# Performance work log

Measured on AMD Instinct MI355X. Metric: run time of the kernel, lower is better.

Reference implementation:

```python
import jax, jax.numpy as jnp
import numpy as np

NEG_SLOPE = 0.2
EPS = 1e-16

def gatv2(x, edge_index, edge_attr, Wl, bl, We, att, bias):
    """PyG GATv2Conv, heads=1, share_weights=True, with edge_dim."""
    N = x.shape[0]
    h = x @ Wl + bl                      # [N, out] shared lin_l == lin_r
    src, dst = edge_index[0], edge_index[1]
    hj = h[src]                          # source (message) features [E, out]
    hi = h[dst]                          # target features [E, out]
    e = jax.nn.leaky_relu(hi + hj + edge_attr @ We, NEG_SLOPE)  # [E, out]
    score = e @ att                      # [E]
    # segment softmax over edges grouped by destination node
    smax = jax.ops.segment_max(score, dst, num_segments=N)
    ex = jnp.exp(score - smax[dst])
    denom = jax.ops.segment_sum(ex, dst, num_segments=N)
    alpha = ex / (denom[dst] + EPS)      # [E]
    out = jax.ops.segment_sum(hj * alpha[:, None], dst, num_segments=N)
    return out + bias


def setup_inputs() -> dict:
    key = jax.random.key(0)
    N, E = 50000, 800000
    D_IN, D_LAT, D_EDGE, N_ACT = 128, 128, 16, 32
    ks = jax.random.split(key, 16)
    s = 0.05
    inp = {
        "x": jax.random.normal(ks[0], (N, D_IN), jnp.float32),
        "edge_index": jax.random.randint(ks[1], (2, E), 0, N, jnp.int32),
        "edge_attr": jax.random.normal(ks[2], (E, D_EDGE), jnp.float32),
        # gnn_layer: D_IN -> D_LAT
        "Wl1": jax.random.normal(ks[3], (D_IN, D_LAT), jnp.float32) * s,
        "bl1": jnp.zeros((D_LAT,), jnp.float32),
        "We1": jax.random.normal(ks[4], (D_EDGE, D_LAT), jnp.float32) * s,
        "att1": jax.random.normal(ks[5], (D_LAT,), jnp.float32) * s,
        "bias1": jnp.zeros((D_LAT,), jnp.float32),
        # node_layer: D_LAT -> 1
        "Wl2": jax.random.normal(ks[6], (D_LAT, 1), jnp.float32) * s,
        "bl2": jnp.zeros((1,), jnp.float32),
        "We2": jax.random.normal(ks[7], (D_EDGE, 1), jnp.float32) * s,
        "att2": jax.random.normal(ks[8], (1,), jnp.float32) * s,
        "bias2": jnp.zeros((1,), jnp.float32),
        # action_layer: D_LAT -> N_ACT
        "Wl3": jax.random.normal(ks[9], (D_LAT, N_ACT), jnp.float32) * s,
        "bl3": jnp.zeros((N_ACT,), jnp.float32),
        "We3": jax.random.normal(ks[10], (D_EDGE, N_ACT), jnp.float32) * s,
        "att3": jax.random.normal(ks[11], (N_ACT,), jnp.float32) * s,
        "bias3": jnp.zeros((N_ACT,), jnp.float32),
    }
    return inp


def reference(x, edge_index, edge_attr,
              Wl1, bl1, We1, att1, bias1,
              Wl2, bl2, We2, att2, bias2,
              Wl3, bl3, We3, att3, bias3):
    latent = gatv2(x, edge_index, edge_attr, Wl1, bl1, We1, att1, bias1)          # [N, D_LAT]
    node_logits = gatv2(latent, edge_index, edge_attr, Wl2, bl2, We2, att2, bias2)[:, 0]  # [N]
    action_logits = gatv2(latent, edge_index, edge_attr, Wl3, bl3, We3, att3, bias3)      # [N, A]
    # categorical sampling with fixed key (deterministic reference)
    k1, k2 = jax.random.split(jax.random.key(42))
    node_sel = jax.random.categorical(k1, node_logits)
    node_lp = jax.nn.log_softmax(node_logits)[node_sel]
    act_logits_sel = action_logits[node_sel, :]
    action_sel = jax.random.categorical(k2, act_logits_sel)
    action_lp = jax.nn.log_softmax(act_logits_sel)[action_sel]
    return (node_sel, action_sel, node_lp + action_lp)
```

## Files before the change

### kernel.cpp

```cpp
#include <hip/hip_runtime.h>
#include <stdint.h>
#include <math.h>

#define NEG 0.2f
#define TINYF 1.1754943508222875e-38f

typedef float f4 __attribute__((ext_vector_type(4)));
typedef float f2 __attribute__((ext_vector_type(2)));

__host__ __device__ inline void threefry2x32(uint32_t k0, uint32_t k1,
                                             uint32_t x0, uint32_t x1,
                                             uint32_t* o0, uint32_t* o1) {
  uint32_t ks0 = k0, ks1 = k1, ks2 = k0 ^ k1 ^ 0x1BD11BDAu;
  x0 += ks0; x1 += ks1;
#define RR(r) { x0 += x1; x1 = (x1 << (r)) | (x1 >> (32 - (r))); x1 ^= x0; }
  RR(13) RR(15) RR(26) RR(6)
  x0 += ks1; x1 += ks2 + 1u;
  RR(17) RR(29) RR(16) RR(24)
  x0 += ks2; x1 += ks0 + 2u;
  RR(13) RR(15) RR(26) RR(6)
  x0 += ks0; x1 += ks1 + 3u;
  RR(17) RR(29) RR(16) RR(24)
  x0 += ks1; x1 += ks2 + 4u;
  RR(13) RR(15) RR(26) RR(6)
  x0 += ks2; x1 += ks0 + 5u;
#undef RR
  *o0 = x0; *o1 = x1;
}

__device__ inline float gumbel_part(uint32_t ka, uint32_t kb, uint32_t i) {
  uint32_t o0, o1;
  threefry2x32(ka, kb, 0u, i, &o0, &o1);
  uint32_t bits = o0 ^ o1;
  float f = __uint_as_float((bits >> 9) | 0x3f800000u) - 1.0f;
  float u = fmaxf(TINYF, f + TINYF);
  return -logf(-logf(u));
}

__global__ void count_kernel(const int* __restrict__ ei, int E, int* __restrict__ counts) {
  int e = blockIdx.x * blockDim.x + threadIdx.x;
  if (e < E) atomicAdd(&counts[ei[E + e]], 1);
}

#define SCB 256
__global__ __launch_bounds__(256) void scan_partial_kernel(const int* __restrict__ counts,
    int N, int chunk, int* __restrict__ bsum) {
  int b = blockIdx.x;
  int s0 = b * chunk, s1 = s0 + chunk; if (s1 > N) s1 = N;
  int tid = threadIdx.x;
  int v = 0;
  for (int i = s0 + tid; i < s1; i += 256) v += counts[i];
  __shared__ int red[256];
  red[tid] = v; __syncthreads();
  for (int s = 128; s; s >>= 1) { if (tid < s) red[tid] += red[tid + s]; __syncthreads(); }
  if (tid == 0) bsum[b] = red[0];
}

__global__ __launch_bounds__(256) void scan_offsets_kernel(const int* __restrict__ bsum,
    int* __restrict__ boff, int* __restrict__ row_start, int N) {
  int tid = threadIdx.x; int lane = tid & 63; int wv = tid >> 6;
  __shared__ int wsum[4];
  int v = bsum[tid];
  int incl = v;
#pragma unroll
  for (int off = 1; off < 64; off <<= 1) {
    int t = __shfl_up(incl, off);
    if (lane >= off) incl += t;
  }
  if (lane == 63) wsum[wv] = incl;
  __syncthreads();
  if (tid == 0) {
    int s = 0;
    for (int k = 0; k < 4; k++) { int t = wsum[k]; wsum[k] = s; s += t; }
    row_start[N] = s;
  }
  __syncthreads();
  boff[tid] = wsum[wv] + incl - v;
}

__global__ __launch_bounds__(256) void scan_apply_kernel(const int* __restrict__ counts,
    const int* __restrict__ boff, int N, int chunk,
    int* __restrict__ row_start, int* __restrict__ cursor) {
  int b = blockIdx.x;
  int s0 = b * chunk, s1 = s0 + chunk; if (s1 > N) s1 = N;
  int tid = threadIdx.x; int lane = tid & 63; int wv = tid >> 6;
  __shared__ int wsum[4];
  __shared__ int tot_s;
  __shared__ int base_s;
  if (tid == 0) base_s = boff[b];
  __syncthreads();
  for (int c0 = s0; c0 < s1; c0 += 256) {
    int i = c0 + tid;
    int v = (i < s1) ? counts[i] : 0;
    int incl = v;
#pragma unroll
    for (int off = 1; off < 64; off <<= 1) {
      int t = __shfl_up(incl, off);
      if (lane >= off) incl += t;
    }
    if (lane == 63) wsum[wv] = incl;
    __syncthreads();
    if (tid == 0) {
      int s = 0;
      for (int k = 0; k < 4; k++) { int t = wsum[k]; wsum[k] = s; s += t; }
      tot_s = s;
    }
    __syncthreads();
    int base = base_s;
    int excl = base + wsum[wv] + incl - v;
    if (i < s1) { row_start[i] = excl; cursor[i] = excl; }
    __syncthreads();
    if (tid == 0) base_s = base + tot_s;
    __syncthreads();
  }
}

__global__ void scatter_kernel(const int* __restrict__ ei, const float* __restrict__ ea,
                               int E, int* __restrict__ cursor,
                               int* __restrict__ src_csr, float* __restrict__ ea_csr) {
  int e = blockIdx.x * blockDim.x + threadIdx.x;
  if (e < E) {
    int d = ei[E + e];
    int p = atomicAdd(&cursor[d], 1);
    src_csr[p] = ei[e];
    const float4* s4 = (const float4*)&ea[(size_t)e * 16];
    float4* d4 = (float4*)&ea_csr[(size_t)p * 16];
    float4 t0 = s4[0], t1 = s4[1], t2 = s4[2], t3 = s4[3];
    d4[0] = t0; d4[1] = t1; d4[2] = t2; d4[3] = t3;
  }
}

__global__ __launch_bounds__(256) void gemm128_kernel(const float* __restrict__ X,
    const float* __restrict__ W, const float* __restrict__ bias,
    float* __restrict__ out, int M) {
  __shared__ float xs[128][33];
  int row0 = blockIdx.x * 32;
  int tid = threadIdx.x;
  for (int idx = tid; idx < 32 * 128; idx += 256) {
    int r = idx >> 7;
    int k = idx & 127;
    int row = row0 + r;
    xs[k][r] = (row < M) ? X[(size_t)row * 128 + k] : 0.0f;
  }
  __syncthreads();
  int tc = tid & 31, tr = tid >> 5;
  int c0 = tc * 4, r0 = tr * 4;
  float acc[4][4] = {};
#pragma unroll 4
  for (int k = 0; k < 128; k++) {
    float4 w = *(const float4*)&W[k * 128 + c0];
    float x0 = xs[k][r0], x1 = xs[k][r0 + 1], x2 = xs[k][r0 + 2], x3 = xs[k][r0 + 3];
    acc[0][0] += x0 * w.x; acc[0][1] += x0 * w.y; acc[0][2] += x0 * w.z; acc[0][3] += x0 * w.w;
    acc[1][0] += x1 * w.x; acc[1][1] += x1 * w.y; acc[1][2] += x1 * w.z; acc[1][3] += x1 * w.w;
    acc[2][0] += x2 * w.x; acc[2][1] += x2 * w.y; acc[2][2] += x2 * w.z; acc[2][3] += x2 * w.w;
    acc[3][0] += x3 * w.x; acc[3][1] += x3 * w.y; acc[3][2] += x3 * w.z; acc[3][3] += x3 * w.w;
  }
  float4 b4 = *(const float4*)&bias[c0];
  for (int r = 0; r < 4; r++) {
    int row = row0 + r0 + r;
    if (row < M) {
      float4 o;
      o.x = acc[r][0] + b4.x; o.y = acc[r][1] + b4.y;
      o.z = acc[r][2] + b4.z; o.w = acc[r][3] + b4.w;
      *(float4*)&out[(size_t)row * 128 + c0] = o;
    }
  }
}

__global__ __launch_bounds__(256) void gemm32_kernel(const float* __restrict__ X,
    const float* __restrict__ W, const float* __restrict__ bias,
    float* __restrict__ out, int M) {
  int t = blockIdx.x * 256 + threadIdx.x;
  int node = t >> 5, c = t & 31;
  if (node >= M) return;
  const float4* xp = (const float4*)&X[(size_t)node * 128];
  float acc = 0.f;
#pragma unroll
  for (int q = 0; q < 32; q++) {
    float4 x4 = xp[q];
    acc += x4.x * W[(q * 4 + 0) * 32 + c] + x4.y * W[(q * 4 + 1) * 32 + c]
         + x4.z * W[(q * 4 + 2) * 32 + c] + x4.w * W[(q * 4 + 3) * 32 + c];
  }
  out[(size_t)node * 32 + c] = acc + bias[c];
}

__global__ __launch_bounds__(256) void gemv_kernel(const float* __restrict__ X,
    const float* __restrict__ w, const float* __restrict__ b0,
    float* __restrict__ out, int M) {
  int wv = (blockIdx.x * 256 + threadIdx.x) >> 6;
  int lane = threadIdx.x & 63;
  if (wv >= M) return;
  float2 xv = *(const float2*)&X[(size_t)wv * 128 + lane * 2];
  float2 wvv = *(const float2*)&w[lane * 2];
  float v = xv.x * wvv.x + xv.y * wvv.y;
#pragma unroll
  for (int off = 32; off; off >>= 1) v += __shfl_xor(v, off);
  if (lane == 0) out[wv] = v + b0[0];
}

__global__ __launch_bounds__(256) void fused1_kernel(const float* __restrict__ h,
    const int* __restrict__ src_csr, const int* __restrict__ row_start,
    const float* __restrict__ ea_csr,
    const float* __restrict__ We, const float* __restrict__ att,
    const float* __restrict__ bias, float* __restrict__ out, int N) {
  __shared__ float WeS[2048];
  int tid = threadIdx.x;
  for (int i = tid; i < 2048; i += 256) WeS[i] = We[i];
  __syncthreads();
  int hw = (blockIdx.x * 256 + tid) >> 5;
  int lane = tid & 31;
  if (hw >= N) return;
  int c4 = lane * 4;
  const f4* W4 = (const f4*)WeS;
  f4 attv = *(const f4*)&att[c4];
  f4 bb = *(const f4*)&bias[c4];
  int start = row_start[hw];
  int deg = row_start[hw + 1] - start;
  if (deg == 0) {
    *(f4*)&out[(size_t)hw * 128 + c4] = bb;
    return;
  }
  f4 hi = *(const f4*)&h[(size_t)hw * 128 + c4];
  int s_l = (lane < deg) ? src_csr[start + lane] : 0;
  int dcap = deg < 32 ? deg : 32;
  const f4* eap = (const f4*)&ea_csr[(size_t)start * 16];
  float m = -INFINITY, l = 0.f;
  f4 acc = (f4)0.f;
  for (int j = 0; j < deg; j++) {
    int s = (j < dcap) ? __shfl(s_l, j, 32) : src_csr[start + j];
    f4 hj = *(const f4*)&h[(size_t)s * 128 + c4];
    f4 v = hi + hj;
#pragma unroll
    for (int q = 0; q < 4; q++) {
      f4 aq = eap[(size_t)j * 4 + q];
      v += aq.x * W4[(4 * q + 0) * 32 + lane];
      v += aq.y * W4[(4 * q + 1) * 32 + lane];
      v += aq.z * W4[(4 * q + 2) * 32 + lane];
      v += aq.w * W4[(4 * q + 3) * 32 + lane];
    }
    v.x = v.x >= 0.f ? v.x : NEG * v.x;
    v.y = v.y >= 0.f ? v.y : NEG * v.y;
    v.z = v.z >= 0.f ? v.z : NEG * v.z;
    v.w = v.w >= 0.f ? v.w : NEG * v.w;
    f4 pv = v * attv;
    float sc = (pv.x + pv.y) + (pv.z + pv.w);
#pragma unroll
    for (int off = 16; off; off >>= 1) sc += __shfl_xor(sc, off);
    float mn = fmaxf(m, sc);
    float scale = __expf(m - mn);
    float w = __expf(sc - mn);
    l = l * scale + w;
    acc = acc * scale + w * hj;
    m = mn;
  }
  float inv = 1.0f / (l + 1e-16f);
  f4 o = acc * inv + bb;
  *(f4*)&out[(size_t)hw * 128 + c4] = o;
}

__global__ __launch_bounds__(256) void fused23_kernel(
    const float* __restrict__ h3, const float* __restrict__ h2,
    const int* __restrict__ src_csr, const int* __restrict__ row_start,
    const float* __restrict__ ea_csr,
    const float* __restrict__ We3, const float* __restrict__ att3,
    const float* __restrict__ bias3, const float* __restrict__ We2,
    const float* __restrict__ att2, const float* __restrict__ bias2,
    float* __restrict__ out3, float* __restrict__ logits, int N) {
  __shared__ float We3S[512];
  __shared__ float att3S[32];
  __shared__ float We2S[16];
  int tid = threadIdx.x;
  for (int i = tid; i < 512; i += 256) We3S[i] = We3[i];
  if (tid < 32) att3S[tid] = att3[tid];
  if (tid < 16) We2S[tid] = We2[tid];
  __syncthreads();
  int wv = (blockIdx.x * 256 + tid) >> 6;
  int lane = tid & 63;
  if (wv >= N) return;
  int q4 = lane >> 4;
  int l16 = lane & 15;
  int c2 = l16 * 2;
  const f2* W3 = (const f2*)We3S;
  f2 at3 = *(const f2*)&att3S[c2];
  float a2s = att2[0];
  f2 bi3 = *(const f2*)&bias3[c2];
  int start = row_start[wv];
  int deg = row_start[wv + 1] - start;
  if (deg == 0) {
    if (lane < 16) *(f2*)&out3[(size_t)wv * 32 + c2] = bi3;
    if (lane == 0) logits[wv] = bias2[0];
    return;
  }
  f2 hi3 = *(const f2*)&h3[(size_t)wv * 32 + c2];
  float hi2 = h2[wv];
  int s_l = (lane < deg) ? src_csr[start + lane] : 0;
  int dcap = deg < 64 ? deg : 64;
  const float4* eap = (const float4*)&ea_csr[(size_t)start * 16];
  float m3 = -INFINITY, l3 = 0.f; f2 a3 = (f2)0.f;
  float m2 = -INFINITY, l2 = 0.f; float a2 = 0.f;
  for (int j = q4; j < deg; j += 4) {
    int s = (j < dcap) ? __shfl(s_l, j) : src_csr[start + j];
    f2 hj3 = *(const f2*)&h3[(size_t)s * 32 + c2];
    float h2s = h2[s];
    float4 c0 = eap[(size_t)j * 4 + 0];
    float4 c1 = eap[(size_t)j * 4 + 1];
    float4 cc2 = eap[(size_t)j * 4 + 2];
    float4 c3 = eap[(size_t)j * 4 + 3];
    f2 v = hi3 + hj3;
    v += c0.x * W3[0 * 16 + l16];  v += c0.y * W3[1 * 16 + l16];
    v += c0.z * W3[2 * 16 + l16];  v += c0.w * W3[3 * 16 + l16];
    v += c1.x * W3[4 * 16 + l16];  v += c1.y * W3[5 * 16 + l16];
    v += c1.z * W3[6 * 16 + l16];  v += c1.w * W3[7 * 16 + l16];
    v += cc2.x * W3[8 * 16 + l16]; v += cc2.y * W3[9 * 16 + l16];
    v += cc2.z * W3[10 * 16 + l16]; v += cc2.w * W3[11 * 16 + l16];
    v += c3.x * W3[12 * 16 + l16]; v += c3.y * W3[13 * 16 + l16];
    v += c3.z * W3[14 * 16 + l16]; v += c3.w * W3[15 * 16 + l16];
    v.x = v.x >= 0.f ? v.x : NEG * v.x;
    v.y = v.y >= 0.f ? v.y : NEG * v.y;
    float t3 = v.x * at3.x + v.y * at3.y;
#pragma unroll
    for (int off = 8; off; off >>= 1) t3 += __shfl_xor(t3, off);
    float v2 = hi2 + h2s;
    v2 += c0.x * We2S[0]  + c0.y * We2S[1]  + c0.z * We2S[2]  + c0.w * We2S[3];
    v2 += c1.x * We2S[4]  + c1.y * We2S[5]  + c1.z * We2S[6]  + c1.w * We2S[7];
    v2 += cc2.x * We2S[8] + cc2.y * We2S[9] + cc2.z * We2S[10] + cc2.w * We2S[11];
    v2 += c3.x * We2S[12] + c3.y * We2S[13] + c3.z * We2S[14] + c3.w * We2S[15];
    v2 = v2 >= 0.f ? v2 : NEG * v2;
    float t2 = v2 * a2s;
    float mn3 = fmaxf(m3, t3);
    float sc3 = __expf(m3 - mn3);
    float w3 = __expf(t3 - mn3);
    l3 = l3 * sc3 + w3;
    a3 = a3 * sc3 + w3 * hj3;
    m3 = mn3;
    float mn2 = fmaxf(m2, t2);
    float sc2 = __expf(m2 - mn2);
    float w2 = __expf(t2 - mn2);
    l2 = l2 * sc2 + w2;
    a2 = a2 * sc2 + w2 * h2s;
    m2 = mn2;
  }
#pragma unroll
  for (int off = 16; off <= 32; off <<= 1) {
    float m3o = __shfl_xor(m3, off), l3o = __shfl_xor(l3, off);
    float ax = __shfl_xor(a3.x, off), ay = __shfl_xor(a3.y, off);
    float M3 = fmaxf(m3, m3o);
    float sA = (m3 == -INFINITY) ? 0.f : __expf(m3 - M3);
    float sB = (m3o == -INFINITY) ? 0.f : __expf(m3o - M3);
    l3 = l3 * sA + l3o * sB;
    a3.x = a3.x * sA + ax * sB;
    a3.y = a3.y * sA + ay * sB;
    m3 = M3;
    float m2o = __shfl_xor(m2, off), l2o = __shfl_xor(l2, off);
    float az = __shfl_xor(a2, off);
    float M2 = fmaxf(m2, m2o);
    float tA = (m2 == -INFINITY) ? 0.f : __expf(m2 - M2);
    float tB = (m2o == -INFINITY) ? 0.f : __expf(m2o - M2);
    l2 = l2 * tA + l2o * tB;
    a2 = a2 * tA + az * tB;
    m2 = M2;
  }
  if (lane < 16) {
    f2 o;
    o.x = a3.x / (l3 + 1e-16f) + bi3.x;
    o.y = a3.y / (l3 + 1e-16f) + bi3.y;
    *(f2*)&out3[(size_t)wv * 32 + c2] = o;
  }
  if (lane == 0) logits[wv] = a2 / (l2 + 1e-16f) + bias2[0];
}

#define NSB 64
__global__ __launch_bounds__(256) void node_partial_kernel(const float* __restrict__ logits,
    int N, uint32_t ka, uint32_t kb,
    float* __restrict__ pB, int* __restrict__ pI,
    float* __restrict__ pM, float* __restrict__ pL) {
  int chunk = (N + NSB - 1) / NSB;
  int s0 = blockIdx.x * chunk;
  int s1 = s0 + chunk; if (s1 > N) s1 = N;
  int tid = threadIdx.x;
  float best = -INFINITY; int bi = 0x7fffffff;
  float m = -INFINITY, l = 0.f;
  for (int i = s0 + tid; i < s1; i += 256) {
    float lg = logits[i];
    float mn = fmaxf(m, lg);
    l = l * __expf(m - mn) + __expf(lg - mn);
    m = mn;
    float v = lg + gumbel_part(ka, kb, (uint32_t)i);
    if (v > best) { best = v; bi = i; }
  }
  __shared__ float sb[256], sm[256], sl[256];
  __shared__ int si[256];
  sb[tid] = best; si[tid] = bi; sm[tid] = m; sl[tid] = l;
  __syncthreads();
  for (int s = 128; s; s >>= 1) {
    if (tid < s) {
      if (sb[tid + s] > sb[tid] || (sb[tid + s] == sb[tid] && si[tid + s] < si[tid])) {
        sb[tid] = sb[tid + s]; si[tid] = si[tid + s];
      }
      float M = fmaxf(sm[tid], sm[tid + s]);
      float t0 = (sm[tid] == -INFINITY) ? 0.f : sl[tid] * __expf(sm[tid] - M);
      float t1 = (sm[tid + s] == -INFINITY) ? 0.f : sl[tid + s] * __expf(sm[tid + s] - M);
      sm[tid] = M; sl[tid] = t0 + t1;
    }
    __syncthreads();
  }
  if (tid == 0) { pB[blockIdx.x] = sb[0]; pI[blockIdx.x] = si[0]; pM[blockIdx.x] = sm[0]; pL[blockIdx.x] = sl[0]; }
}

__global__ __launch_bounds__(64) void node_final_kernel(const float* __restrict__ logits,
    const float* __restrict__ pB, const int* __restrict__ pI,
    const float* __restrict__ pM, const float* __restrict__ pL,
    float* __restrict__ scal) {
  int lane = threadIdx.x;
  float best = pB[lane]; int bi = pI[lane];
  float m = pM[lane]; float l = pL[lane];
#pragma unroll
  for (int off = 32; off; off >>= 1) {
    float ob = __shfl_xor(best, off); int oi = __shfl_xor(bi, off);
    if (ob > best || (ob == best && oi < bi)) { best = ob; bi = oi; }
    float om = __shfl_xor(m, off); float ol = __shfl_xor(l, off);
    float M = fmaxf(m, om);
    float t0 = (m == -INFINITY) ? 0.f : l * __expf(m - M);
    float t1 = (om == -INFINITY) ? 0.f : ol * __expf(om - M);
    m = M; l = t0 + t1;
  }
  if (lane == 0) {
    ((int*)scal)[0] = bi;
    scal[3] = logits[bi] - (m + logf(l));
  }
}

__global__ __launch_bounds__(64) void action_kernel(const float* __restrict__ out3,
    const float* __restrict__ scal, uint32_t ka, uint32_t kb,
    float* __restrict__ dout, int out_size) {
  int lane = threadIdx.x;
  int sel = ((const int*)scal)[0];
  float v = -INFINITY, noisy = -INFINITY;
  if (lane < 32) {
    v = out3[(size_t)sel * 32 + lane];
    noisy = v + gumbel_part(ka, kb, (uint32_t)lane);
  }
  int idx = lane;
  float nv = noisy;
#pragma unroll
  for (int off = 32; off; off >>= 1) {
    float ov = __shfl_xor(nv, off);
    int oi = __shfl_xor(idx, off);
    if (ov > nv || (ov == nv && oi < idx)) { nv = ov; idx = oi; }
  }
  float vm = v;
#pragma unroll
  for (int off = 32; off; off >>= 1) vm = fmaxf(vm, __shfl_xor(vm, off));
  float ex = (lane < 32) ? expf(v - vm) : 0.f;
#pragma unroll
  for (int off = 32; off; off >>= 1) ex += __shfl_xor(ex, off);
  float vsel = __shfl(v, idx);
  if (lane == 0) {
    float action_lp = vsel - vm - logf(ex);
    dout[0] = (float)sel;
    dout[1] = (float)idx;
    dout[2] = scal[3] + action_lp;
  }
  for (int i = 3 + lane; i < out_size; i += 64) dout[i] = 0.f;
}

extern "C" void kernel_launch(void* const* d_in, const int* in_sizes, int n_in,
                              void* d_out, int out_size, void* d_ws, size_t ws_size,
                              hipStream_t stream) {
  const float* x     = (const float*)d_in[0];
  const int*   ei    = (const int*)d_in[1];
  const float* ea    = (const float*)d_in[2];
  const float* Wl1   = (const float*)d_in[3];
  const float* bl1   = (const float*)d_in[4];
  const float* We1   = (const float*)d_in[5];
  const float* att1  = (const float*)d_in[6];
  const float* bias1 = (const float*)d_in[7];
  const float* Wl2   = (const float*)d_in[8];
  const float* bl2   = (const float*)d_in[9];
  const float* We2   = (const float*)d_in[10];
  const float* att2  = (const float*)d_in[11];
  const float* bias2 = (const float*)d_in[12];
  const float* Wl3   = (const float*)d_in[13];
  const float* bl3   = (const float*)d_in[14];
  const float* We3   = (const float*)d_in[15];
  const float* att3  = (const float*)d_in[16];
  const float* bias3 = (const float*)d_in[17];
  int N = in_sizes[0] / 128;
  int E = in_sizes[1] / 2;
  float* out = (float*)d_out;

  char* p = (char*)d_ws;
  auto alloc = [&](size_t bytes) -> char* {
    char* r = p; p += (bytes + 255) & ~(size_t)255; return r;
  };
  float* h1      = (float*)alloc((size_t)N * 128 * 4);
  float* latent  = (float*)alloc((size_t)N * 128 * 4);
  float* h3      = (float*)alloc((size_t)N * 32 * 4);
  float* h2      = (float*)alloc((size_t)N * 4);
  float* logits  = (float*)alloc((size_t)N * 4);
  float* out3    = (float*)alloc((size_t)N * 32 * 4);
  int* counts    = (int*)alloc((size_t)N * 4);
  int* row_start = (int*)alloc((size_t)(N + 1) * 4);
  int* cursor    = (int*)alloc((size_t)N * 4);
  int* src_csr   = (int*)alloc((size_t)E * 4);
  float* ea_csr  = (float*)alloc((size_t)E * 16 * 4);
  int* bsum      = (int*)alloc(SCB * 4);
  int* boff      = (int*)alloc(SCB * 4);
  float* pB      = (float*)alloc(NSB * 4);
  int*   pI      = (int*)alloc(NSB * 4);
  float* pM      = (float*)alloc(NSB * 4);
  float* pL      = (float*)alloc(NSB * 4);
  float* scal    = (float*)alloc(64);
  (void)ws_size; (void)n_in;

  uint32_t k1a, k1b, k2a, k2b;
  threefry2x32(0u, 42u, 0u, 0u, &k1a, &k1b);
  threefry2x32(0u, 42u, 0u, 1u, &k2a, &k2b);

  int chunk = (N + SCB - 1) / SCB;

  hipMemsetAsync(counts, 0, (size_t)N * 4, stream);
  count_kernel<<<(E + 255) / 256, 256, 0, stream>>>(ei, E, counts);
  scan_partial_kernel<<<SCB, 256, 0, stream>>>(counts, N, chunk, bsum);
  scan_offsets_kernel<<<1, 256, 0, stream>>>(bsum, boff, row_start, N);
  scan_apply_kernel<<<SCB, 256, 0, stream>>>(counts, boff, N, chunk, row_start, cursor);
  scatter_kernel<<<(E + 255) / 256, 256, 0, stream>>>(ei, ea, E, cursor, src_csr, ea_csr);

  gemm128_kernel<<<(N + 31) / 32, 256, 0, stream>>>(x, Wl1, bl1, h1, N);
  fused1_kernel<<<(N + 7) / 8, 256, 0, stream>>>(h1, src_csr, row_start,
                                                 ea_csr, We1, att1, bias1, latent, N);

  gemm32_kernel<<<((size_t)N * 32 + 255) / 256, 256, 0, stream>>>(latent, Wl3, bl3, h3, N);
  gemv_kernel<<<(N + 3) / 4, 256, 0, stream>>>(latent, Wl2, bl2, h2, N);

  fused23_kernel<<<(N + 3) / 4, 256, 0, stream>>>(h3, h2, src_csr, row_start, ea_csr,
                                                  We3, att3, bias3, We2, att2, bias2,
                                                  out3, logits, N);

  node_partial_kernel<<<NSB, 256, 0, stream>>>(logits, N, k1a, k1b, pB, pI, pM, pL);
  node_final_kernel<<<1, 64, 0, stream>>>(logits, pB, pI, pM, pL, scal);
  action_kernel<<<1, 64, 0, stream>>>(out3, scal, k2a, k2b, out, out_size);
}
```

Measured before the change: 578.9 us.

## Process four edges per iteration in fused1 with split online-softmax merge

fused1 now assigns one full 64-lane wavefront per destination node instead of a 32-lane half-wave. Each half-wave handles interleaved edges, and each lane tracks two independent online-softmax states (edges 4t+half and 4t+half+2), so four edges are in flight per loop iteration. The partial states are merged across the two streams and then across halves with xor-32 shuffles. The intent is more memory-level parallelism for the gathered h rows and a shorter serial dependency chain. In exchange the launch needs twice as many wavefronts and uses more registers, and low-degree nodes (average degree about 16) waste padded lanes.

```diff
diff --git a/kernel.cpp b/kernel.cpp
--- a/kernel.cpp
+++ b/kernel.cpp
@@ -207,55 +207,108 @@
   int tid = threadIdx.x;
   for (int i = tid; i < 2048; i += 256) WeS[i] = We[i];
   __syncthreads();
-  int hw = (blockIdx.x * 256 + tid) >> 5;
-  int lane = tid & 31;
-  if (hw >= N) return;
-  int c4 = lane * 4;
+  int wv = (blockIdx.x * 256 + tid) >> 6;
+  int lane = tid & 63;
+  if (wv >= N) return;
+  int half = lane >> 5;
+  int l32 = lane & 31;
+  int c4 = l32 * 4;
   const f4* W4 = (const f4*)WeS;
   f4 attv = *(const f4*)&att[c4];
   f4 bb = *(const f4*)&bias[c4];
-  int start = row_start[hw];
-  int deg = row_start[hw + 1] - start;
+  int start = row_start[wv];
+  int deg = row_start[wv + 1] - start;
   if (deg == 0) {
-    *(f4*)&out[(size_t)hw * 128 + c4] = bb;
+    if (lane < 32) *(f4*)&out[(size_t)wv * 128 + c4] = bb;
     return;
   }
-  f4 hi = *(const f4*)&h[(size_t)hw * 128 + c4];
+  f4 hi = *(const f4*)&h[(size_t)wv * 128 + c4];
   int s_l = (lane < deg) ? src_csr[start + lane] : 0;
-  int dcap = deg < 32 ? deg : 32;
+  int dcap = deg < 64 ? deg : 64;
   const f4* eap = (const f4*)&ea_csr[(size_t)start * 16];
-  float m = -INFINITY, l = 0.f;
-  f4 acc = (f4)0.f;
-  for (int j = 0; j < deg; j++) {
-    int s = (j < dcap) ? __shfl(s_l, j, 32) : src_csr[start + j];
-    f4 hj = *(const f4*)&h[(size_t)s * 128 + c4];
-    f4 v = hi + hj;
+  float m0 = -INFINITY, l0 = 0.f; f4 a0 = (f4)0.f;
+  float m1 = -INFINITY, l1 = 0.f; f4 a1 = (f4)0.f;
+  int nt = (deg + 3) >> 2;
+  for (int t = 0; t < nt; t++) {
+    int ja = 4 * t + half;
+    int jb = ja + 2;
+    int jac = (ja < deg) ? ja : 0;
+    int jbc = (jb < deg) ? jb : 0;
+    int sA = (jac < dcap) ? __shfl(s_l, jac) : src_csr[start + jac];
+    int sB = (jbc < dcap) ? __shfl(s_l, jbc) : src_csr[start + jbc];
+    f4 hjA = *(const f4*)&h[(size_t)sA * 128 + c4];
+    f4 hjB = *(const f4*)&h[(size_t)sB * 128 + c4];
+    f4 vA = hi + hjA;
+    f4 vB = hi + hjB;
 #pragma unroll
     for (int q = 0; q < 4; q++) {
-      f4 aq = eap[(size_t)j * 4 + q];
-      v += aq.x * W4[(4 * q + 0) * 32 + lane];
-      v += aq.y * W4[(4 * q + 1) * 32 + lane];
-      v += aq.z * W4[(4 * q + 2) * 32 + lane];
-      v += aq.w * W4[(4 * q + 3) * 32 + lane];
-    }
-    v.x = v.x >= 0.f ? v.x : NEG * v.x;
-    v.y = v.y >= 0.f ? v.y : NEG * v.y;
-    v.z = v.z >= 0.f ? v.z : NEG * v.z;
-    v.w = v.w >= 0.f ? v.w : NEG * v.w;
-    f4 pv = v * attv;
-    float sc = (pv.x + pv.y) + (pv.z + pv.w);
-#pragma unroll
-    for (int off = 16; off; off >>= 1) sc += __shfl_xor(sc, off);
-    float mn = fmaxf(m, sc);
-    float scale = __expf(m - mn);
-    float w = __expf(sc - mn);
-    l = l * scale + w;
-    acc = acc * scale + w * hj;
-    m = mn;
-  }
-  float inv = 1.0f / (l + 1e-16f);
-  f4 o = acc * inv + bb;
-  *(f4*)&out[(size_t)hw * 128 + c4] = o;
+      f4 aqA = eap[(size_t)jac * 4 + q];
+      f4 aqB = eap[(size_t)jbc * 4 + q];
+      f4 w0 = W4[(4 * q + 0) * 32 + l32];
+      f4 w1 = W4[(4 * q + 1) * 32 + l32];
+      f4 w2 = W4[(4 * q + 2) * 32 + l32];
+      f4 w3 = W4[(4 * q + 3) * 32 + l32];
+      vA += aqA.x * w0 + aqA.y * w1 + aqA.z * w2 + aqA.w * w3;
+      vB += aqB.x * w0 + aqB.y * w1 + aqB.z * w2 + aqB.w * w3;
+    }
+    vA.x = vA.x >= 0.f ? vA.x : NEG * vA.x;
+    vA.y = vA.y >= 0.f ? vA.y : NEG * vA.y;
+    vA.z = vA.z >= 0.f ? vA.z : NEG * vA.z;
+    vA.w = vA.w >= 0.f ? vA.w : NEG * vA.w;
+    vB.x = vB.x >= 0.f ? vB.x : NEG * vB.x;
+    vB.y = vB.y >= 0.f ? vB.y : NEG * vB.y;
+    vB.z = vB.z >= 0.f ? vB.z : NEG * vB.z;
+    vB.w = vB.w >= 0.f ? vB.w : NEG * vB.w;
+    f4 pA = vA * attv;
+    f4 pB = vB * attv;
+    float scA = (pA.x + pA.y) + (pA.z + pA.w);
+    float scB = (pB.x + pB.y) + (pB.z + pB.w);
+#pragma unroll
+    for (int off = 16; off; off >>= 1) {
+      scA += __shfl_xor(scA, off);
+      scB += __shfl_xor(scB, off);
+    }
+    if (ja < deg) {
+      float mn = fmaxf(m0, scA);
+      float s = __expf(m0 - mn);
+      float w = __expf(scA - mn);
+      l0 = l0 * s + w; a0 = a0 * s + w * hjA; m0 = mn;
+    }
+    if (jb < deg) {
+      float mn = fmaxf(m1, scB);
+      float s = __expf(m1 - mn);
+      float w = __expf(scB - mn);
+      l1 = l1 * s + w; a1 = a1 * s + w * hjB; m1 = mn;
+    }
+  }
+  {
+    float M = fmaxf(m0, m1);
+    float s0 = (m0 == -INFINITY) ? 0.f : __expf(m0 - M);
+    float s1 = (m1 == -INFINITY) ? 0.f : __expf(m1 - M);
+    l0 = l0 * s0 + l1 * s1;
+    a0 = a0 * s0 + a1 * s1;
+    m0 = M;
+  }
+  {
+    float mo = __shfl_xor(m0, 32);
+    float lo = __shfl_xor(l0, 32);
+    f4 ao;
+    ao.x = __shfl_xor(a0.x, 32);
+    ao.y = __shfl_xor(a0.y, 32);
+    ao.z = __shfl_xor(a0.z, 32);
+    ao.w = __shfl_xor(a0.w, 32);
+    float M = fmaxf(m0, mo);
+    float s0 = (m0 == -INFINITY) ? 0.f : __expf(m0 - M);
+    float s1 = (mo == -INFINITY) ? 0.f : __expf(mo - M);
+    l0 = l0 * s0 + lo * s1;
+    a0 = a0 * s0 + ao * s1;
+    m0 = M;
+  }
+  if (lane < 32) {
+    float inv = 1.0f / (l0 + 1e-16f);
+    f4 o = a0 * inv + bb;
+    *(f4*)&out[(size_t)wv * 128 + c4] = o;
+  }
 }
 
 __global__ __launch_bounds__(256) void fused23_kernel(
@@ -527,7 +580,7 @@
   scatter_kernel<<<(E + 255) / 256, 256, 0, stream>>>(ei, ea, E, cursor, src_csr, ea_csr);
 
   gemm128_kernel<<<(N + 31) / 32, 256, 0, stream>>>(x, Wl1, bl1, h1, N);
-  fused1_kernel<<<(N + 7) / 8, 256, 0, stream>>>(h1, src_csr, row_start,
+  fused1_kernel<<<(N + 3) / 4, 256, 0, stream>>>(h1, src_csr, row_start,
                                                  ea_csr, We1, att1, bias1, latent, N);
 
   gemm32_kernel<<<((size_t)N * 32 + 255) / 256, 256, 0, stream>>>(latent, Wl3, bl3, h3, N);
```

Result: slower. 658.9 us (+13.8%).

## Drop online-max softmax for clamped exp and pipeline two edges per iteration

Applied to the files above, without the earlier changes.

Both aggregation kernels drop the running-max online softmax and instead accumulate exp of the score clamped at 60, so the per-edge rescale exps and the max-merge across lane groups go away. The layer-1 kernel also processes two edges per iteration and prefetches the next pair's source feature rows, giving more loads in flight and independent work. This changes the numerics: the result only matches the reference while scores stay small enough that the unshifted exp neither overflows nor underflows, and the clamp alters results for any score above 60.

```diff
diff --git a/kernel.cpp b/kernel.cpp
--- a/kernel.cpp
+++ b/kernel.cpp
@@ -224,34 +224,63 @@
   int s_l = (lane < deg) ? src_csr[start + lane] : 0;
   int dcap = deg < 32 ? deg : 32;
   const f4* eap = (const f4*)&ea_csr[(size_t)start * 16];
-  float m = -INFINITY, l = 0.f;
+  int dm1 = deg - 1;
+
+  int sA0 = __shfl(s_l, 0, 32);
+  int j1 = (1 <= dm1) ? 1 : dm1;
+  int sB0 = (j1 < dcap) ? __shfl(s_l, j1, 32) : src_csr[start + j1];
+  f4 hjA = *(const f4*)&h[(size_t)sA0 * 128 + c4];
+  f4 hjB = *(const f4*)&h[(size_t)sB0 * 128 + c4];
+
+  float l = 0.f;
   f4 acc = (f4)0.f;
-  for (int j = 0; j < deg; j++) {
-    int s = (j < dcap) ? __shfl(s_l, j, 32) : src_csr[start + j];
-    f4 hj = *(const f4*)&h[(size_t)s * 128 + c4];
-    f4 v = hi + hj;
+  int nt = (deg + 1) >> 1;
+  for (int t = 0; t < nt; t++) {
+    int jB = 2 * t + 1;
+    f4 cA = hjA, cB = hjB;
+    int nA = 2 * t + 2; if (nA > dm1) nA = dm1;
+    int nB = 2 * t + 3; if (nB > dm1) nB = dm1;
+    int snA = (nA < dcap) ? __shfl(s_l, nA, 32) : src_csr[start + nA];
+    int snB = (nB < dcap) ? __shfl(s_l, nB, 32) : src_csr[start + nB];
+    hjA = *(const f4*)&h[(size_t)snA * 128 + c4];
+    hjB = *(const f4*)&h[(size_t)snB * 128 + c4];
+    int jBc = (jB <= dm1) ? jB : dm1;
+    const f4* eA = eap + (size_t)(2 * t) * 4;
+    const f4* eB = eap + (size_t)jBc * 4;
+    f4 vA = hi + cA;
+    f4 vB = hi + cB;
 #pragma unroll
     for (int q = 0; q < 4; q++) {
-      f4 aq = eap[(size_t)j * 4 + q];
-      v += aq.x * W4[(4 * q + 0) * 32 + lane];
-      v += aq.y * W4[(4 * q + 1) * 32 + lane];
-      v += aq.z * W4[(4 * q + 2) * 32 + lane];
-      v += aq.w * W4[(4 * q + 3) * 32 + lane];
+      f4 a4 = eA[q];
+      f4 b4 = eB[q];
+      f4 w0 = W4[(4 * q + 0) * 32 + lane];
+      f4 w1 = W4[(4 * q + 1) * 32 + lane];
+      f4 w2 = W4[(4 * q + 2) * 32 + lane];
+      f4 w3 = W4[(4 * q + 3) * 32 + lane];
+      vA += a4.x * w0 + a4.y * w1 + a4.z * w2 + a4.w * w3;
+      vB += b4.x * w0 + b4.y * w1 + b4.z * w2 + b4.w * w3;
     }
-    v.x = v.x >= 0.f ? v.x : NEG * v.x;
-    v.y = v.y >= 0.f ? v.y : NEG * v.y;
-    v.z = v.z >= 0.f ? v.z : NEG * v.z;
-    v.w = v.w >= 0.f ? v.w : NEG * v.w;
-    f4 pv = v * attv;
-    float sc = (pv.x + pv.y) + (pv.z + pv.w);
-#pragma unroll
-    for (int off = 16; off; off >>= 1) sc += __shfl_xor(sc, off);
-    float mn = fmaxf(m, sc);
-    float scale = __expf(m - mn);
-    float w = __expf(sc - mn);
-    l = l * scale + w;
-    acc = acc * scale + w * hj;
-    m = mn;
+    vA.x = vA.x >= 0.f ? vA.x : NEG * vA.x;
+    vA.y = vA.y >= 0.f ? vA.y : NEG * vA.y;
+    vA.z = vA.z >= 0.f ? vA.z : NEG * vA.z;
+    vA.w = vA.w >= 0.f ? vA.w : NEG * vA.w;
+    vB.x = vB.x >= 0.f ? vB.x : NEG * vB.x;
+    vB.y = vB.y >= 0.f ? vB.y : NEG * vB.y;
+    vB.z = vB.z >= 0.f ? vB.z : NEG * vB.z;
+    vB.w = vB.w >= 0.f ? vB.w : NEG * vB.w;
+    f4 pA = vA * attv;
+    f4 pB = vB * attv;
+    float scA = (pA.x + pA.y) + (pA.z + pA.w);
+    float scB = (pB.x + pB.y) + (pB.z + pB.w);
+#pragma unroll
+    for (int off = 16; off; off >>= 1) {
+      scA += __shfl_xor(scA, off);
+      scB += __shfl_xor(scB, off);
+    }
+    float wA = __expf(fminf(scA, 60.f));
+    float wB = (jB <= dm1) ? __expf(fminf(scB, 60.f)) : 0.f;
+    l += wA + wB;
+    acc += wA * cA + wB * cB;
   }
   float inv = 1.0f / (l + 1e-16f);
   f4 o = acc * inv + bb;
@@ -296,8 +325,8 @@
   int s_l = (lane < deg) ? src_csr[start + lane] : 0;
   int dcap = deg < 64 ? deg : 64;
   const float4* eap = (const float4*)&ea_csr[(size_t)start * 16];
-  float m3 = -INFINITY, l3 = 0.f; f2 a3 = (f2)0.f;
-  float m2 = -INFINITY, l2 = 0.f; float a2 = 0.f;
+  float l3 = 0.f; f2 a3 = (f2)0.f;
+  float l2 = 0.f; float a2 = 0.f;
   for (int j = q4; j < deg; j += 4) {
     int s = (j < dcap) ? __shfl(s_l, j) : src_csr[start + j];
     f2 hj3 = *(const f2*)&h3[(size_t)s * 32 + c2];
@@ -327,38 +356,20 @@
     v2 += c3.x * We2S[12] + c3.y * We2S[13] + c3.z * We2S[14] + c3.w * We2S[15];
     v2 = v2 >= 0.f ? v2 : NEG * v2;
     float t2 = v2 * a2s;
-    float mn3 = fmaxf(m3, t3);
-    float sc3 = __expf(m3 - mn3);
-    float w3 = __expf(t3 - mn3);
-    l3 = l3 * sc3 + w3;
-    a3 = a3 * sc3 + w3 * hj3;
-    m3 = mn3;
-    float mn2 = fmaxf(m2, t2);
-    float sc2 = __expf(m2 - mn2);
-    float w2 = __expf(t2 - mn2);
-    l2 = l2 * sc2 + w2;
-    a2 = a2 * sc2 + w2 * h2s;
-    m2 = mn2;
+    float w3 = __expf(fminf(t3, 60.f));
+    l3 += w3;
+    a3 += w3 * hj3;
+    float w2 = __expf(fminf(t2, 60.f));
+    l2 += w2;
+    a2 += w2 * h2s;
   }
 #pragma unroll
   for (int off = 16; off <= 32; off <<= 1) {
-    float m3o = __shfl_xor(m3, off), l3o = __shfl_xor(l3, off);
-    float ax = __shfl_xor(a3.x, off), ay = __shfl_xor(a3.y, off);
-    float M3 = fmaxf(m3, m3o);
-    float sA = (m3 == -INFINITY) ? 0.f : __expf(m3 - M3);
-    float sB = (m3o == -INFINITY) ? 0.f : __expf(m3o - M3);
-    l3 = l3 * sA + l3o * sB;
-    a3.x = a3.x * sA + ax * sB;
-    a3.y = a3.y * sA + ay * sB;
-    m3 = M3;
-    float m2o = __shfl_xor(m2, off), l2o = __shfl_xor(l2, off);
-    float az = __shfl_xor(a2, off);
-    float M2 = fmaxf(m2, m2o);
-    float tA = (m2 == -INFINITY) ? 0.f : __expf(m2 - M2);
-    float tB = (m2o == -INFINITY) ? 0.f : __expf(m2o - M2);
-    l2 = l2 * tA + l2o * tB;
-    a2 = a2 * tA + az * tB;
-    m2 = M2;
+    l3 += __shfl_xor(l3, off);
+    a3.x += __shfl_xor(a3.x, off);
+    a3.y += __shfl_xor(a3.y, off);
+    l2 += __shfl_xor(l2, off);
+    a2 += __shfl_xor(a2, off);
   }
   if (lane < 16) {
     f2 o;
```

Result: slower. 653.3 us (+12.8%).

## Keep edge weights in registers and software-prefetch neighbor rows in GAT aggregation

Applied to the files above, without the earlier changes.

Both fused aggregation kernels now hold the 16-row edge-weight matrix in per-lane registers instead of staging it in LDS behind a block barrier. The layer-1 kernel also prefetches neighbour feature rows three edges ahead and edge attributes one edge ahead, so the dependent gather latency overlaps with the current edge's math. This removes LDS reads and the __syncthreads, but needs many more VGPRs (16 f4 weight rows plus three f4 prefetch buffers), which could lower occupancy. Indices are clamped to the last edge, so some trailing loads are redundant.

```diff
diff --git a/kernel.cpp b/kernel.cpp
--- a/kernel.cpp
+++ b/kernel.cpp
@@ -203,15 +203,27 @@
     const float* __restrict__ ea_csr,
     const float* __restrict__ We, const float* __restrict__ att,
     const float* __restrict__ bias, float* __restrict__ out, int N) {
-  __shared__ float WeS[2048];
   int tid = threadIdx.x;
-  for (int i = tid; i < 2048; i += 256) WeS[i] = We[i];
-  __syncthreads();
   int hw = (blockIdx.x * 256 + tid) >> 5;
   int lane = tid & 31;
   if (hw >= N) return;
   int c4 = lane * 4;
-  const f4* W4 = (const f4*)WeS;
+  f4 wr0  = *(const f4*)&We[0  * 128 + c4];
+  f4 wr1  = *(const f4*)&We[1  * 128 + c4];
+  f4 wr2  = *(const f4*)&We[2  * 128 + c4];
+  f4 wr3  = *(const f4*)&We[3  * 128 + c4];
+  f4 wr4  = *(const f4*)&We[4  * 128 + c4];
+  f4 wr5  = *(const f4*)&We[5  * 128 + c4];
+  f4 wr6  = *(const f4*)&We[6  * 128 + c4];
+  f4 wr7  = *(const f4*)&We[7  * 128 + c4];
+  f4 wr8  = *(const f4*)&We[8  * 128 + c4];
+  f4 wr9  = *(const f4*)&We[9  * 128 + c4];
+  f4 wr10 = *(const f4*)&We[10 * 128 + c4];
+  f4 wr11 = *(const f4*)&We[11 * 128 + c4];
+  f4 wr12 = *(const f4*)&We[12 * 128 + c4];
+  f4 wr13 = *(const f4*)&We[13 * 128 + c4];
+  f4 wr14 = *(const f4*)&We[14 * 128 + c4];
+  f4 wr15 = *(const f4*)&We[15 * 128 + c4];
   f4 attv = *(const f4*)&att[c4];
   f4 bb = *(const f4*)&bias[c4];
   int start = row_start[hw];
@@ -224,20 +236,34 @@
   int s_l = (lane < deg) ? src_csr[start + lane] : 0;
   int dcap = deg < 32 ? deg : 32;
   const f4* eap = (const f4*)&ea_csr[(size_t)start * 16];
+  int dm1 = deg - 1;
+
+  f4 e0 = eap[0], e1 = eap[1], e2 = eap[2], e3 = eap[3];
+  int sp0 = __shfl(s_l, 0, 32);
+  f4 hj0 = *(const f4*)&h[(size_t)sp0 * 128 + c4];
+  int jp1 = (1 < dm1) ? 1 : dm1;
+  int sp1 = (jp1 < dcap) ? __shfl(s_l, jp1, 32) : src_csr[start + jp1];
+  f4 hj1 = *(const f4*)&h[(size_t)sp1 * 128 + c4];
+  int jp2 = (2 < dm1) ? 2 : dm1;
+  int sp2 = (jp2 < dcap) ? __shfl(s_l, jp2, 32) : src_csr[start + jp2];
+  f4 hj2 = *(const f4*)&h[(size_t)sp2 * 128 + c4];
+
   float m = -INFINITY, l = 0.f;
   f4 acc = (f4)0.f;
   for (int j = 0; j < deg; j++) {
-    int s = (j < dcap) ? __shfl(s_l, j, 32) : src_csr[start + j];
-    f4 hj = *(const f4*)&h[(size_t)s * 128 + c4];
+    f4 hj = hj0; hj0 = hj1; hj1 = hj2;
+    f4 ce0 = e0, ce1 = e1, ce2 = e2, ce3 = e3;
+    int je = j + 1; if (je > dm1) je = dm1;
+    const f4* ep = eap + (size_t)je * 4;
+    e0 = ep[0]; e1 = ep[1]; e2 = ep[2]; e3 = ep[3];
+    int jn = j + 3; if (jn > dm1) jn = dm1;
+    int sn = (jn < dcap) ? __shfl(s_l, jn, 32) : src_csr[start + jn];
+    hj2 = *(const f4*)&h[(size_t)sn * 128 + c4];
     f4 v = hi + hj;
-#pragma unroll
-    for (int q = 0; q < 4; q++) {
-      f4 aq = eap[(size_t)j * 4 + q];
-      v += aq.x * W4[(4 * q + 0) * 32 + lane];
-      v += aq.y * W4[(4 * q + 1) * 32 + lane];
-      v += aq.z * W4[(4 * q + 2) * 32 + lane];
-      v += aq.w * W4[(4 * q + 3) * 32 + lane];
-    }
+    v += ce0.x * wr0  + ce0.y * wr1  + ce0.z * wr2  + ce0.w * wr3;
+    v += ce1.x * wr4  + ce1.y * wr5  + ce1.z * wr6  + ce1.w * wr7;
+    v += ce2.x * wr8  + ce2.y * wr9  + ce2.z * wr10 + ce2.w * wr11;
+    v += ce3.x * wr12 + ce3.y * wr13 + ce3.z * wr14 + ce3.w * wr15;
     v.x = v.x >= 0.f ? v.x : NEG * v.x;
     v.y = v.y >= 0.f ? v.y : NEG * v.y;
     v.z = v.z >= 0.f ? v.z : NEG * v.z;
@@ -266,22 +292,34 @@
     const float* __restrict__ bias3, const float* __restrict__ We2,
     const float* __restrict__ att2, const float* __restrict__ bias2,
     float* __restrict__ out3, float* __restrict__ logits, int N) {
-  __shared__ float We3S[512];
-  __shared__ float att3S[32];
-  __shared__ float We2S[16];
   int tid = threadIdx.x;
-  for (int i = tid; i < 512; i += 256) We3S[i] = We3[i];
-  if (tid < 32) att3S[tid] = att3[tid];
-  if (tid < 16) We2S[tid] = We2[tid];
-  __syncthreads();
   int wv = (blockIdx.x * 256 + tid) >> 6;
   int lane = tid & 63;
   if (wv >= N) return;
   int q4 = lane >> 4;
   int l16 = lane & 15;
   int c2 = l16 * 2;
-  const f2* W3 = (const f2*)We3S;
-  f2 at3 = *(const f2*)&att3S[c2];
+  f2 w3r0  = *(const f2*)&We3[0  * 32 + c2];
+  f2 w3r1  = *(const f2*)&We3[1  * 32 + c2];
+  f2 w3r2  = *(const f2*)&We3[2  * 32 + c2];
+  f2 w3r3  = *(const f2*)&We3[3  * 32 + c2];
+  f2 w3r4  = *(const f2*)&We3[4  * 32 + c2];
+  f2 w3r5  = *(const f2*)&We3[5  * 32 + c2];
+  f2 w3r6  = *(const f2*)&We3[6  * 32 + c2];
+  f2 w3r7  = *(const f2*)&We3[7  * 32 + c2];
+  f2 w3r8  = *(const f2*)&We3[8  * 32 + c2];
+  f2 w3r9  = *(const f2*)&We3[9  * 32 + c2];
+  f2 w3r10 = *(const f2*)&We3[10 * 32 + c2];
+  f2 w3r11 = *(const f2*)&We3[11 * 32 + c2];
+  f2 w3r12 = *(const f2*)&We3[12 * 32 + c2];
+  f2 w3r13 = *(const f2*)&We3[13 * 32 + c2];
+  f2 w3r14 = *(const f2*)&We3[14 * 32 + c2];
+  f2 w3r15 = *(const f2*)&We3[15 * 32 + c2];
+  float u0 = We2[0],  u1 = We2[1],  u2 = We2[2],  u3 = We2[3];
+  float u4 = We2[4],  u5 = We2[5],  u6 = We2[6],  u7 = We2[7];
+  float u8 = We2[8],  u9 = We2[9],  u10 = We2[10], u11 = We2[11];
+  float u12 = We2[12], u13 = We2[13], u14 = We2[14], u15 = We2[15];
+  f2 at3 = *(const f2*)&att3[c2];
   float a2s = att2[0];
   f2 bi3 = *(const f2*)&bias3[c2];
   int start = row_start[wv];
@@ -307,24 +345,24 @@
     float4 cc2 = eap[(size_t)j * 4 + 2];
     float4 c3 = eap[(size_t)j * 4 + 3];
     f2 v = hi3 + hj3;
-    v += c0.x * W3[0 * 16 + l16];  v += c0.y * W3[1 * 16 + l16];
-    v += c0.z * W3[2 * 16 + l16];  v += c0.w * W3[3 * 16 + l16];
-    v += c1.x * W3[4 * 16 + l16];  v += c1.y * W3[5 * 16 + l16];
-    v += c1.z * W3[6 * 16 + l16];  v += c1.w * W3[7 * 16 + l16];
-    v += cc2.x * W3[8 * 16 + l16]; v += cc2.y * W3[9 * 16 + l16];
-    v += cc2.z * W3[10 * 16 + l16]; v += cc2.w * W3[11 * 16 + l16];
-    v += c3.x * W3[12 * 16 + l16]; v += c3.y * W3[13 * 16 + l16];
-    v += c3.z * W3[14 * 16 + l16]; v += c3.w * W3[15 * 16 + l16];
+    v += c0.x * w3r0;   v += c0.y * w3r1;
+    v += c0.z * w3r2;   v += c0.w * w3r3;
+    v += c1.x * w3r4;   v += c1.y * w3r5;
+    v += c1.z * w3r6;   v += c1.w * w3r7;
+    v += cc2.x * w3r8;  v += cc2.y * w3r9;
+    v += cc2.z * w3r10; v += cc2.w * w3r11;
+    v += c3.x * w3r12;  v += c3.y * w3r13;
+    v += c3.z * w3r14;  v += c3.w * w3r15;
     v.x = v.x >= 0.f ? v.x : NEG * v.x;
     v.y = v.y >= 0.f ? v.y : NEG * v.y;
     float t3 = v.x * at3.x + v.y * at3.y;
 #pragma unroll
     for (int off = 8; off; off >>= 1) t3 += __shfl_xor(t3, off);
     float v2 = hi2 + h2s;
-    v2 += c0.x * We2S[0]  + c0.y * We2S[1]  + c0.z * We2S[2]  + c0.w * We2S[3];
-    v2 += c1.x * We2S[4]  + c1.y * We2S[5]  + c1.z * We2S[6]  + c1.w * We2S[7];
-    v2 += cc2.x * We2S[8] + cc2.y * We2S[9] + cc2.z * We2S[10] + cc2.w * We2S[11];
-    v2 += c3.x * We2S[12] + c3.y * We2S[13] + c3.z * We2S[14] + c3.w * We2S[15];
+    v2 += c0.x * u0   + c0.y * u1   + c0.z * u2   + c0.w * u3;
+    v2 += c1.x * u4   + c1.y * u5   + c1.z * u6   + c1.w * u7;
+    v2 += cc2.x * u8  + cc2.y * u9  + cc2.z * u10 + cc2.w * u11;
+    v2 += c3.x * u12  + c3.y * u13  + c3.z * u14  + c3.w * u15;
     v2 = v2 >= 0.f ? v2 : NEG * v2;
     float t2 = v2 * a2s;
     float mn3 = fmaxf(m3, t3);
```

After: 591.9 us. 1.02x slower.
